# Performance work log

Hardware: AMD Instinct MI355X
Metric: run time of the kernel (lower is better)

## Reference

```python
import jax, jax.numpy as jnp
import numpy as np

ALPHA = 0.2  # LeakyReLU negative slope
NEG_INF = -9e15  # matches torch's -9000000000000000.0


def setup_inputs() -> dict:
    key = jax.random.key(0)
    k1, k2, k3, k4 = jax.random.split(key, 4)
    B, T, N, F_in, D = 4, 32, 512, 128, 128
    h = jax.random.normal(k1, (B, T, N, F_in), dtype=jnp.float32)
    adj = jax.random.randint(k2, (N, N), 0, 2, dtype=jnp.int32)
    # params: W ~ Linear(in_dim, out_dim, bias=False); a ~ Linear(2*out_dim, 1, bias=False)
    W = jax.random.normal(k3, (F_in, D), dtype=jnp.float32) * 0.05
    a = jax.random.normal(k4, (2 * D,), dtype=jnp.float32) * 0.05
    return {"h": h, "adj": adj, "W": W, "a": a}


def reference(h, adj, W, a):
    # h: (B,T,N,F_in), adj: (N,N), W: (F_in,D), a: (2D,)
    D = W.shape[1]
    Wh = jnp.einsum('btnf,fd->btnd', h, W)  # (B,T,N,D)
    # a . [Wh_i ; Wh_j] == a_src . Wh_i + a_dst . Wh_j -- avoids (N,N,2D) concat
    a_src, a_dst = a[:D], a[D:]
    e_src = Wh @ a_src  # (B,T,N)
    e_dst = Wh @ a_dst  # (B,T,N)
    e = jax.nn.leaky_relu(e_src[..., :, None] + e_dst[..., None, :], ALPHA)  # (B,T,N,N)
    e = jnp.where(adj > 0, e, jnp.float32(NEG_INF))
    attention = jax.nn.softmax(e, axis=-1)  # dropout is identity at eval
    h_prime = jnp.einsum('btij,btjd->btid', attention, Wh)  # (B,T,N,D)
    return h_prime
```

## Files before the change

kernel.cpp:

```cpp
#include <hip/hip_runtime.h>
#include <math.h>

typedef __attribute__((ext_vector_type(8))) short bf16x8;
typedef __attribute__((ext_vector_type(4))) float f32x4;

#define MFMA(a, b, c) __builtin_amdgcn_mfma_f32_16x16x32_bf16(a, b, c, 0, 0, 0)

constexpr int GN = 128;
constexpr int NN = 512;
constexpr int FD = 128;
#define LRELU(x) fmaxf((x), 0.2f * (x))
#define NEG_BIG -9.0e15f

__device__ inline unsigned short bf16_rne(float x) {
    unsigned u = __float_as_uint(x);
    unsigned r = u + 0x7fffu + ((u >> 16) & 1u);
    return (unsigned short)(r >> 16);
}
__device__ inline float bf16_to_f(unsigned short h) {
    return __uint_as_float(((unsigned)h) << 16);
}
__device__ inline unsigned rne_top16(float x) {
    unsigned u = __float_as_uint(x);
    return u + 0x7fffu + ((u >> 16) & 1u);
}
__device__ inline unsigned pack_top16(unsigned e1, unsigned e0) {
    return __builtin_amdgcn_perm(e1, e0, 0x07060302u);
}
__device__ inline void gload16(const void* g, void* l) {
    __builtin_amdgcn_global_load_lds(
        (const __attribute__((address_space(1))) unsigned*)g,
        (__attribute__((address_space(3))) unsigned*)l, 16, 0, 0);
}
__device__ inline void decode_bid(int bid, int& g, int& tile) {
    const int xcd = bid & 7, slot = bid >> 3;
    g = xcd + 8 * (slot >> 2);
    tile = slot & 3;
}

__global__ __launch_bounds__(256) void prep_kernel(
    const int* __restrict__ adj, const float* __restrict__ W,
    unsigned* __restrict__ mask, unsigned short* __restrict__ wsHi,
    unsigned short* __restrict__ wsLo)
{
    const int b = blockIdx.x, t = threadIdx.x;
    if (b < 32) {
        const int wi = b * 256 + t;
        const int row = wi >> 4, wo = wi & 15;
        const int* p = adj + row * NN + wo * 32;
        unsigned m = 0;
        #pragma unroll
        for (int q = 0; q < 32; q += 4) {
            int4 v = *(const int4*)&p[q];
            m |= (v.x > 0 ? 1u : 0u) << q;
            m |= (v.y > 0 ? 1u : 0u) << (q + 1);
            m |= (v.z > 0 ? 1u : 0u) << (q + 2);
            m |= (v.w > 0 ? 1u : 0u) << (q + 3);
        }
        mask[wi] = m;
    } else {
        const int base = (b - 32) * 512 + t * 2;
        #pragma unroll
        for (int q = 0; q < 2; ++q) {
            const int pos = base + q;
            const int idx = pos & 7, lane = (pos >> 3) & 63, cn = pos >> 9;
            const int kk = cn >> 3, nb = cn & 7;
            const int k = kk * 32 + ((lane >> 4) & 3) * 8 + idx;
            const int d = nb * 16 + (lane & 15);
            const float wv = W[k * FD + d];
            const unsigned u = __float_as_uint(wv);
            wsHi[pos] = (unsigned short)(u >> 16);
            wsLo[pos] = (unsigned short)(rne_top16(
                            wv - __uint_as_float(u & 0xffff0000u)) >> 16);
        }
    }
}

__global__ __launch_bounds__(256, 3) void whb_kernel(
    const float* __restrict__ h, const float* __restrict__ a,
    const unsigned short* __restrict__ wsHi, const unsigned short* __restrict__ wsLo,
    unsigned short* __restrict__ whtHi, unsigned short* __restrict__ whtLo,
    float* __restrict__ esrc, float* __restrict__ edst)
{
    __shared__ __attribute__((aligned(16))) unsigned short sBuf[16384];
    unsigned short* sWhi = sBuf;
    unsigned short* sWlo = sBuf + 4096;
    float* hs = (float*)(sBuf + 8192);

    int g, jt;
    decode_bid(blockIdx.x, g, jt);
    const int t = threadIdx.x, lane = t & 63, w = t >> 6;
    const int i0r = jt * 128;
    const float* hg = h + (size_t)(g * NN) * FD;

    f32x4 acc[2][8];
    #pragma unroll
    for (int mt = 0; mt < 2; ++mt)
        #pragma unroll
        for (int nb = 0; nb < 8; ++nb) acc[mt][nb] = (f32x4){0.f, 0.f, 0.f, 0.f};

    for (int kk = 0; kk < 4; ++kk) {
        __syncthreads();
        for (int q = t; q < 512; q += 256) {
            gload16(&wsHi[kk * 4096 + q * 8], &sWhi[q * 8]);
            gload16(&wsLo[kk * 4096 + q * 8], &sWlo[q * 8]);
        }
        for (int q = t; q < 1024; q += 256) {
            const int w2 = q >> 8, mt = (q >> 7) & 1;
            const int lp = (q >> 1) & 63, half = q & 1;
            const int row = i0r + w2 * 32 + mt * 16 + (lp & 15);
            const int k = kk * 32 + ((lp >> 4) & 3) * 8 + half * 4;
            gload16(hg + (size_t)row * FD + k, &hs[q * 4]);
        }
        __syncthreads();

        bf16x8 ah[2], al[2];
        #pragma unroll
        for (int mt = 0; mt < 2; ++mt) {
            const float* fb = &hs[((w * 2 + mt) * 64 + lane) * 8];
            const float4 f0 = *(const float4*)fb;
            const float4 f1 = *(const float4*)(fb + 4);
            const float xs[8] = {f0.x, f0.y, f0.z, f0.w, f1.x, f1.y, f1.z, f1.w};
            union { bf16x8 v; unsigned u[4]; } H, L;
            #pragma unroll
            for (int j = 0; j < 4; ++j) {
                const unsigned e0 = __float_as_uint(xs[2 * j]);
                const unsigned e1 = __float_as_uint(xs[2 * j + 1]);
                H.u[j] = pack_top16(e1, e0);
                const unsigned l0 = rne_top16(xs[2*j]   - __uint_as_float(e0 & 0xffff0000u));
                const unsigned l1 = rne_top16(xs[2*j+1] - __uint_as_float(e1 & 0xffff0000u));
                L.u[j] = pack_top16(l1, l0);
            }
            ah[mt] = H.v; al[mt] = L.v;
        }
        #pragma unroll
        for (int nb = 0; nb < 8; ++nb) {
            const bf16x8 bh = *(const bf16x8*)&sWhi[(nb * 64 + lane) * 8];
            const bf16x8 bl = *(const bf16x8*)&sWlo[(nb * 64 + lane) * 8];
            #pragma unroll
            for (int mt = 0; mt < 2; ++mt) {
                acc[mt][nb] = MFMA(al[mt], bh, acc[mt][nb]);
                acc[mt][nb] = MFMA(ah[mt], bl, acc[mt][nb]);
                acc[mt][nb] = MFMA(ah[mt], bh, acc[mt][nb]);
            }
        }
    }

    float av[8], bv[8];
    #pragma unroll
    for (int nb = 0; nb < 8; ++nb) {
        av[nb] = a[nb * 16 + (lane & 15)];
        bv[nb] = a[FD + nb * 16 + (lane & 15)];
    }
    #pragma unroll
    for (int mt = 0; mt < 2; ++mt)
        #pragma unroll
        for (int r = 0; r < 4; ++r) {
            float ps = 0.f, pd = 0.f;
            #pragma unroll
            for (int nb = 0; nb < 8; ++nb) {
                ps += acc[mt][nb][r] * av[nb];
                pd += acc[mt][nb][r] * bv[nb];
            }
            #pragma unroll
            for (int off = 1; off <= 8; off <<= 1) {
                ps += __shfl_xor(ps, off);
                pd += __shfl_xor(pd, off);
            }
            if ((lane & 15) == 0) {
                const int row = g * NN + i0r + w * 32 + mt * 16 + (lane >> 4) * 4 + r;
                esrc[row] = ps;
                edst[row] = pd;
            }
        }

    unsigned short* sTh = sBuf;
    unsigned short* sTl = sBuf + 8192;
    const size_t gbase = (size_t)g * 65536 + (size_t)jt * 16384;
    const int lanep = (lane & 15) + 16 * ((lane >> 5) + 0);
    const int ib = 4 * ((lane >> 4) & 1);

    for (int ph = 0; ph < 2; ++ph) {
        __syncthreads();
        #pragma unroll
        for (int mt = 0; mt < 2; ++mt) {
            const int lp2 = (lane & 15) + 16 * (mt * 2 + (lane >> 5));
            #pragma unroll
            for (int nbp = 0; nbp < 4; ++nbp) {
                const int nb = ph * 4 + nbp;
                const int off = ((w * 4 + nbp) * 64 + lp2) * 8 + ib;
                const unsigned u0 = __float_as_uint(acc[mt][nb][0]);
                const unsigned u1 = __float_as_uint(acc[mt][nb][1]);
                const unsigned u2 = __float_as_uint(acc[mt][nb][2]);
                const unsigned u3 = __float_as_uint(acc[mt][nb][3]);
                *(uint2*)&sTh[off] = make_uint2(pack_top16(u1, u0), pack_top16(u3, u2));
                const unsigned l0 = rne_top16(acc[mt][nb][0] - __uint_as_float(u0 & 0xffff0000u));
                const unsigned l1 = rne_top16(acc[mt][nb][1] - __uint_as_float(u1 & 0xffff0000u));
                const unsigned l2 = rne_top16(acc[mt][nb][2] - __uint_as_float(u2 & 0xffff0000u));
                const unsigned l3 = rne_top16(acc[mt][nb][3] - __uint_as_float(u3 & 0xffff0000u));
                *(uint2*)&sTl[off] = make_uint2(pack_top16(l1, l0), pack_top16(l3, l2));
            }
        }
        __syncthreads();
        for (int q = t; q < 1024; q += 256) {
            const int qw = q >> 8, qr = q & 255;
            const size_t go = gbase + (size_t)(qw * 8 + ph * 4) * 512 + qr * 8;
            *(float4*)&whtHi[go] = *(const float4*)&sTh[q * 8];
            *(float4*)&whtLo[go] = *(const float4*)&sTl[q * 8];
        }
    }
    (void)lanep;
}

__global__ __launch_bounds__(256, 3) void attn_kernel(
    const unsigned short* __restrict__ whtHi, const unsigned short* __restrict__ whtLo,
    const float* __restrict__ esrc, const float* __restrict__ edst,
    const unsigned* __restrict__ mask, float* __restrict__ out)
{
    __shared__ __attribute__((aligned(16))) float eds[NN];
    __shared__ __attribute__((aligned(16))) unsigned maskS[2048];
    __shared__ __attribute__((aligned(16))) unsigned short cHi[8192];
    __shared__ __attribute__((aligned(16))) unsigned short cLo[8192];
    __shared__ float redS[4];

    int g, it;
    decode_bid(blockIdx.x, g, it);
    const int t = threadIdx.x, lane = t & 63, w = t >> 6;
    const int i0 = it * 128;
    const int q8 = (lane >> 4) * 8;

    const float e0 = edst[g * NN + t], e1 = edst[g * NN + 256 + t];
    eds[t] = e0; eds[t + 256] = e1;
    float mx = fmaxf(e0, e1);
    #pragma unroll
    for (int off = 1; off < 64; off <<= 1) mx = fmaxf(mx, __shfl_xor(mx, off));
    if (lane == 0) redS[w] = mx;
    *(uint4*)&maskS[t * 8]     = *(const uint4*)&mask[i0 * 16 + t * 8];
    *(uint4*)&maskS[t * 8 + 4] = *(const uint4*)&mask[i0 * 16 + t * 8 + 4];
    __syncthreads();
    const float maxE = fmaxf(fmaxf(redS[0], redS[1]), fmaxf(redS[2], redS[3]));

    const int rloc0 = w * 32 + (lane & 15);
    const int rloc1 = rloc0 + 16;
    const float s0 = esrc[g * NN + i0 + rloc0];
    const float s1 = esrc[g * NN + i0 + rloc1];
    const float mh0 = LRELU(s0 + maxE);
    const float mh1 = LRELU(s1 + maxE);

    f32x4 acc[2][8];
    #pragma unroll
    for (int mt = 0; mt < 2; ++mt)
        #pragma unroll
        for (int nb = 0; nb < 8; ++nb) acc[mt][nb] = (f32x4){0.f, 0.f, 0.f, 0.f};
    float lsum0 = 0.f, lsum1 = 0.f;

    for (int c2 = 0; c2 < 8; ++c2) {
        __syncthreads();
        const size_t gb = (size_t)g * 65536 + (size_t)c2 * 8192;
        for (int q = t; q < 1024; q += 256) {
            gload16(&whtHi[gb + q * 8], &cHi[q * 8]);
            gload16(&whtLo[gb + q * 8], &cLo[q * 8]);
        }
        __syncthreads();
        #pragma unroll
        for (int kl = 0; kl < 2; ++kl) {
            const int kk = c2 * 2 + kl;
            const float* ep = &eds[kk * 32 + q8];
            const float4 ed0 = *(const float4*)ep;
            const float4 ed1 = *(const float4*)(ep + 4);
            const float ev[8] = {ed0.x, ed0.y, ed0.z, ed0.w, ed1.x, ed1.y, ed1.z, ed1.w};
            const unsigned mw0 = maskS[rloc0 * 16 + kk] >> q8;
            const unsigned mw1 = maskS[rloc1 * 16 + kk] >> q8;

            union { bf16x8 v; unsigned u[4]; } H0, L0, H1, L1;
            unsigned uh[8], ul[8];
            #pragma unroll
            for (int i = 0; i < 8; ++i) {
                float x = s0 + ev[i];
                x = LRELU(x);
                x = ((mw0 >> i) & 1u) ? x : NEG_BIG;
                const float p = __expf(x - mh0);
                lsum0 += p;
                const unsigned u = __float_as_uint(p);
                uh[i] = u;
                ul[i] = rne_top16(p - __uint_as_float(u & 0xffff0000u));
            }
            #pragma unroll
            for (int j = 0; j < 4; ++j) {
                H0.u[j] = pack_top16(uh[2*j+1], uh[2*j]);
                L0.u[j] = pack_top16(ul[2*j+1], ul[2*j]);
            }
            #pragma unroll
            for (int i = 0; i < 8; ++i) {
                float x = s1 + ev[i];
                x = LRELU(x);
                x = ((mw1 >> i) & 1u) ? x : NEG_BIG;
                const float p = __expf(x - mh1);
                lsum1 += p;
                const unsigned u = __float_as_uint(p);
                uh[i] = u;
                ul[i] = rne_top16(p - __uint_as_float(u & 0xffff0000u));
            }
            #pragma unroll
            for (int j = 0; j < 4; ++j) {
                H1.u[j] = pack_top16(uh[2*j+1], uh[2*j]);
                L1.u[j] = pack_top16(ul[2*j+1], ul[2*j]);
            }
            #pragma unroll
            for (int nb = 0; nb < 8; ++nb) {
                const bf16x8 bh = *(const bf16x8*)&cHi[((kl * 8 + nb) * 64 + lane) * 8];
                const bf16x8 bl = *(const bf16x8*)&cLo[((kl * 8 + nb) * 64 + lane) * 8];
                acc[0][nb] = MFMA(L0.v, bh, acc[0][nb]);
                acc[0][nb] = MFMA(H0.v, bl, acc[0][nb]);
                acc[0][nb] = MFMA(H0.v, bh, acc[0][nb]);
                acc[1][nb] = MFMA(L1.v, bh, acc[1][nb]);
                acc[1][nb] = MFMA(H1.v, bl, acc[1][nb]);
                acc[1][nb] = MFMA(H1.v, bh, acc[1][nb]);
            }
        }
    }

    lsum0 += __shfl_xor(lsum0, 16); lsum0 += __shfl_xor(lsum0, 32);
    lsum1 += __shfl_xor(lsum1, 16); lsum1 += __shfl_xor(lsum1, 32);

    #pragma unroll
    for (int r = 0; r < 4; ++r) {
        const int rr = (lane >> 4) * 4 + r;
        const float rl0 = 1.0f / __shfl(lsum0, rr);
        const float rl1 = 1.0f / __shfl(lsum1, rr);
        const int row0 = g * NN + i0 + w * 32 + rr;
        const int row1 = row0 + 16;
        #pragma unroll
        for (int nb = 0; nb < 8; ++nb) {
            out[row0 * FD + nb * 16 + (lane & 15)] = acc[0][nb][r] * rl0;
            out[row1 * FD + nb * 16 + (lane & 15)] = acc[1][nb][r] * rl1;
        }
    }
}

extern "C" void kernel_launch(void* const* d_in, const int* in_sizes, int n_in,
                              void* d_out, int out_size, void* d_ws, size_t ws_size,
                              hipStream_t stream) {
    const float* h   = (const float*)d_in[0];
    const int*   adj = (const int*)d_in[1];
    const float* W   = (const float*)d_in[2];
    const float* a   = (const float*)d_in[3];
    float* out = (float*)d_out;

    unsigned short* whtHi = (unsigned short*)d_ws;
    unsigned short* whtLo = whtHi + (size_t)GN * 65536;
    float* esrc = (float*)(whtLo + (size_t)GN * 65536);
    float* edst = esrc + GN * NN;
    unsigned* mask = (unsigned*)(edst + GN * NN);
    unsigned short* wsHi = (unsigned short*)(mask + 8192);
    unsigned short* wsLo = wsHi + 16384;

    prep_kernel<<<64, 256, 0, stream>>>(adj, W, mask, wsHi, wsLo);
    whb_kernel<<<512, 256, 0, stream>>>(h, a, wsHi, wsLo, whtHi, whtLo, esrc, edst);
    attn_kernel<<<512, 256, 0, stream>>>(whtHi, whtLo, esrc, edst, mask, out);
}
```

Before: 132.8 us.

## Restructure whb and attn kernels: full W in LDS, smaller attn tiles, 2-term split

The whb kernel now stages all of W (hi and lo) into LDS once and reads h straight from global memory into registers, instead of reloading per k-chunk with two barriers each time. The attn kernel halves its row tile to 64 rows per block, doubles the grid to 1024 blocks, and keeps each thread's mask row in registers rather than in LDS. It also drops the low bf16 part of the attention probabilities, going from 3 MFMAs to 2 per product, and sums the rounded probabilities so the normalisation matches. This cuts MFMA count and register pressure so more blocks fit per CU, at the cost of lower precision in the probability operand and more redundant loads of the Wh tiles across blocks.

Measured after the change: 130.7 us. Within noise of the previous version (-1.6%).

```diff
diff --git a/kernel.cpp b/kernel.cpp
--- a/kernel.cpp
+++ b/kernel.cpp
@@ -12,14 +12,6 @@
 #define LRELU(x) fmaxf((x), 0.2f * (x))
 #define NEG_BIG -9.0e15f
 
-__device__ inline unsigned short bf16_rne(float x) {
-    unsigned u = __float_as_uint(x);
-    unsigned r = u + 0x7fffu + ((u >> 16) & 1u);
-    return (unsigned short)(r >> 16);
-}
-__device__ inline float bf16_to_f(unsigned short h) {
-    return __uint_as_float(((unsigned)h) << 16);
-}
 __device__ inline unsigned rne_top16(float x) {
     unsigned u = __float_as_uint(x);
     return u + 0x7fffu + ((u >> 16) & 1u);
@@ -31,11 +23,6 @@
     __builtin_amdgcn_global_load_lds(
         (const __attribute__((address_space(1))) unsigned*)g,
         (__attribute__((address_space(3))) unsigned*)l, 16, 0, 0);
-}
-__device__ inline void decode_bid(int bid, int& g, int& tile) {
-    const int xcd = bid & 7, slot = bid >> 3;
-    g = xcd + 8 * (slot >> 2);
-    tile = slot & 3;
 }
 
 __global__ __launch_bounds__(256) void prep_kernel(
@@ -76,50 +63,44 @@
     }
 }
 
-__global__ __launch_bounds__(256, 3) void whb_kernel(
+__global__ __launch_bounds__(256, 2) void whb_kernel(
     const float* __restrict__ h, const float* __restrict__ a,
     const unsigned short* __restrict__ wsHi, const unsigned short* __restrict__ wsLo,
     unsigned short* __restrict__ whtHi, unsigned short* __restrict__ whtLo,
     float* __restrict__ esrc, float* __restrict__ edst)
 {
-    __shared__ __attribute__((aligned(16))) unsigned short sBuf[16384];
-    unsigned short* sWhi = sBuf;
-    unsigned short* sWlo = sBuf + 4096;
-    float* hs = (float*)(sBuf + 8192);
-
-    int g, jt;
-    decode_bid(blockIdx.x, g, jt);
+    __shared__ __attribute__((aligned(16))) unsigned short sW[32768];
+
+    const int bid = blockIdx.x;
+    const int xcd = bid & 7, slot = bid >> 3;
+    const int g = xcd + 8 * (slot >> 2);
+    const int jt = slot & 3;
     const int t = threadIdx.x, lane = t & 63, w = t >> 6;
     const int i0r = jt * 128;
+    const int q8 = (lane >> 4) * 8;
     const float* hg = h + (size_t)(g * NN) * FD;
 
+    for (int q = t; q < 2048; q += 256) {
+        gload16(&wsHi[q * 8], &sW[q * 8]);
+        gload16(&wsLo[q * 8], &sW[16384 + q * 8]);
+    }
+    __syncthreads();
+
     f32x4 acc[2][8];
     #pragma unroll
     for (int mt = 0; mt < 2; ++mt)
         #pragma unroll
         for (int nb = 0; nb < 8; ++nb) acc[mt][nb] = (f32x4){0.f, 0.f, 0.f, 0.f};
 
+    #pragma unroll
     for (int kk = 0; kk < 4; ++kk) {
-        __syncthreads();
-        for (int q = t; q < 512; q += 256) {
-            gload16(&wsHi[kk * 4096 + q * 8], &sWhi[q * 8]);
-            gload16(&wsLo[kk * 4096 + q * 8], &sWlo[q * 8]);
-        }
-        for (int q = t; q < 1024; q += 256) {
-            const int w2 = q >> 8, mt = (q >> 7) & 1;
-            const int lp = (q >> 1) & 63, half = q & 1;
-            const int row = i0r + w2 * 32 + mt * 16 + (lp & 15);
-            const int k = kk * 32 + ((lp >> 4) & 3) * 8 + half * 4;
-            gload16(hg + (size_t)row * FD + k, &hs[q * 4]);
-        }
-        __syncthreads();
-
         bf16x8 ah[2], al[2];
         #pragma unroll
         for (int mt = 0; mt < 2; ++mt) {
-            const float* fb = &hs[((w * 2 + mt) * 64 + lane) * 8];
-            const float4 f0 = *(const float4*)fb;
-            const float4 f1 = *(const float4*)(fb + 4);
+            const float* src = hg + (size_t)(i0r + w * 32 + mt * 16 + (lane & 15)) * FD
+                             + kk * 32 + q8;
+            const float4 f0 = *(const float4*)src;
+            const float4 f1 = *(const float4*)(src + 4);
             const float xs[8] = {f0.x, f0.y, f0.z, f0.w, f1.x, f1.y, f1.z, f1.w};
             union { bf16x8 v; unsigned u[4]; } H, L;
             #pragma unroll
@@ -135,8 +116,8 @@
         }
         #pragma unroll
         for (int nb = 0; nb < 8; ++nb) {
-            const bf16x8 bh = *(const bf16x8*)&sWhi[(nb * 64 + lane) * 8];
-            const bf16x8 bl = *(const bf16x8*)&sWlo[(nb * 64 + lane) * 8];
+            const bf16x8 bh = *(const bf16x8*)&sW[((kk * 8 + nb) * 64 + lane) * 8];
+            const bf16x8 bl = *(const bf16x8*)&sW[16384 + ((kk * 8 + nb) * 64 + lane) * 8];
             #pragma unroll
             for (int mt = 0; mt < 2; ++mt) {
                 acc[mt][nb] = MFMA(al[mt], bh, acc[mt][nb]);
@@ -174,10 +155,9 @@
             }
         }
 
-    unsigned short* sTh = sBuf;
-    unsigned short* sTl = sBuf + 8192;
+    unsigned short* sTh = sW;
+    unsigned short* sTl = sW + 8192;
     const size_t gbase = (size_t)g * 65536 + (size_t)jt * 16384;
-    const int lanep = (lane & 15) + 16 * ((lane >> 5) + 0);
     const int ib = 4 * ((lane >> 4) & 1);
 
     for (int ph = 0; ph < 2; ++ph) {
@@ -209,24 +189,24 @@
             *(float4*)&whtLo[go] = *(const float4*)&sTl[q * 8];
         }
     }
-    (void)lanep;
-}
-
-__global__ __launch_bounds__(256, 3) void attn_kernel(
+}
+
+__global__ __launch_bounds__(256, 4) void attn_kernel(
     const unsigned short* __restrict__ whtHi, const unsigned short* __restrict__ whtLo,
     const float* __restrict__ esrc, const float* __restrict__ edst,
     const unsigned* __restrict__ mask, float* __restrict__ out)
 {
     __shared__ __attribute__((aligned(16))) float eds[NN];
-    __shared__ __attribute__((aligned(16))) unsigned maskS[2048];
     __shared__ __attribute__((aligned(16))) unsigned short cHi[8192];
     __shared__ __attribute__((aligned(16))) unsigned short cLo[8192];
     __shared__ float redS[4];
 
-    int g, it;
-    decode_bid(blockIdx.x, g, it);
+    const int bid = blockIdx.x;
+    const int xcd = bid & 7, slot = bid >> 3;
+    const int g = xcd + 8 * (slot >> 3);
+    const int it = slot & 7;
     const int t = threadIdx.x, lane = t & 63, w = t >> 6;
-    const int i0 = it * 128;
+    const int i0 = it * 64;
     const int q8 = (lane >> 4) * 8;
 
     const float e0 = edst[g * NN + t], e1 = edst[g * NN + 256 + t];
@@ -235,24 +215,22 @@
     #pragma unroll
     for (int off = 1; off < 64; off <<= 1) mx = fmaxf(mx, __shfl_xor(mx, off));
     if (lane == 0) redS[w] = mx;
-    *(uint4*)&maskS[t * 8]     = *(const uint4*)&mask[i0 * 16 + t * 8];
-    *(uint4*)&maskS[t * 8 + 4] = *(const uint4*)&mask[i0 * 16 + t * 8 + 4];
+
+    const int rloc = w * 16 + (lane & 15);
+    const float s0 = esrc[g * NN + i0 + rloc];
+    unsigned mrow[16];
+    *(uint4*)&mrow[0]  = *(const uint4*)&mask[(i0 + rloc) * 16];
+    *(uint4*)&mrow[4]  = *(const uint4*)&mask[(i0 + rloc) * 16 + 4];
+    *(uint4*)&mrow[8]  = *(const uint4*)&mask[(i0 + rloc) * 16 + 8];
+    *(uint4*)&mrow[12] = *(const uint4*)&mask[(i0 + rloc) * 16 + 12];
     __syncthreads();
     const float maxE = fmaxf(fmaxf(redS[0], redS[1]), fmaxf(redS[2], redS[3]));
-
-    const int rloc0 = w * 32 + (lane & 15);
-    const int rloc1 = rloc0 + 16;
-    const float s0 = esrc[g * NN + i0 + rloc0];
-    const float s1 = esrc[g * NN + i0 + rloc1];
-    const float mh0 = LRELU(s0 + maxE);
-    const float mh1 = LRELU(s1 + maxE);
-
-    f32x4 acc[2][8];
-    #pragma unroll
-    for (int mt = 0; mt < 2; ++mt)
-        #pragma unroll
-        for (int nb = 0; nb < 8; ++nb) acc[mt][nb] = (f32x4){0.f, 0.f, 0.f, 0.f};
-    float lsum0 = 0.f, lsum1 = 0.f;
+    const float mh = LRELU(s0 + maxE);
+
+    f32x4 acc[8];
+    #pragma unroll
+    for (int nb = 0; nb < 8; ++nb) acc[nb] = (f32x4){0.f, 0.f, 0.f, 0.f};
+    float lsum = 0.f;
 
     for (int c2 = 0; c2 < 8; ++c2) {
         __syncthreads();
@@ -269,72 +247,44 @@
             const float4 ed0 = *(const float4*)ep;
             const float4 ed1 = *(const float4*)(ep + 4);
             const float ev[8] = {ed0.x, ed0.y, ed0.z, ed0.w, ed1.x, ed1.y, ed1.z, ed1.w};
-            const unsigned mw0 = maskS[rloc0 * 16 + kk] >> q8;
-            const unsigned mw1 = maskS[rloc1 * 16 + kk] >> q8;
-
-            union { bf16x8 v; unsigned u[4]; } H0, L0, H1, L1;
-            unsigned uh[8], ul[8];
+            const unsigned mw = mrow[kk] >> q8;
+
+            union { bf16x8 v; unsigned u[4]; } H;
+            unsigned uh[8];
             #pragma unroll
             for (int i = 0; i < 8; ++i) {
                 float x = s0 + ev[i];
                 x = LRELU(x);
-                x = ((mw0 >> i) & 1u) ? x : NEG_BIG;
-                const float p = __expf(x - mh0);
-                lsum0 += p;
-                const unsigned u = __float_as_uint(p);
-                uh[i] = u;
-                ul[i] = rne_top16(p - __uint_as_float(u & 0xffff0000u));
-            }
-            #pragma unroll
-            for (int j = 0; j < 4; ++j) {
-                H0.u[j] = pack_top16(uh[2*j+1], uh[2*j]);
-                L0.u[j] = pack_top16(ul[2*j+1], ul[2*j]);
-            }
-            #pragma unroll
-            for (int i = 0; i < 8; ++i) {
-                float x = s1 + ev[i];
-                x = LRELU(x);
-                x = ((mw1 >> i) & 1u) ? x : NEG_BIG;
-                const float p = __expf(x - mh1);
-                lsum1 += p;
-                const unsigned u = __float_as_uint(p);
-                uh[i] = u;
-                ul[i] = rne_top16(p - __uint_as_float(u & 0xffff0000u));
-            }
-            #pragma unroll
-            for (int j = 0; j < 4; ++j) {
-                H1.u[j] = pack_top16(uh[2*j+1], uh[2*j]);
-                L1.u[j] = pack_top16(ul[2*j+1], ul[2*j]);
-            }
+                x = ((mw >> i) & 1u) ? x : NEG_BIG;
+                const float p = __expf(x - mh);
+                const unsigned r = rne_top16(p);
+                lsum += __uint_as_float(r & 0xffff0000u);
+                uh[i] = r;
+            }
+            #pragma unroll
+            for (int j = 0; j < 4; ++j) H.u[j] = pack_top16(uh[2*j+1], uh[2*j]);
+
             #pragma unroll
             for (int nb = 0; nb < 8; ++nb) {
+                const bf16x8 bl = *(const bf16x8*)&cLo[((kl * 8 + nb) * 64 + lane) * 8];
                 const bf16x8 bh = *(const bf16x8*)&cHi[((kl * 8 + nb) * 64 + lane) * 8];
-                const bf16x8 bl = *(const bf16x8*)&cLo[((kl * 8 + nb) * 64 + lane) * 8];
-                acc[0][nb] = MFMA(L0.v, bh, acc[0][nb]);
-                acc[0][nb] = MFMA(H0.v, bl, acc[0][nb]);
-                acc[0][nb] = MFMA(H0.v, bh, acc[0][nb]);
-                acc[1][nb] = MFMA(L1.v, bh, acc[1][nb]);
-                acc[1][nb] = MFMA(H1.v, bl, acc[1][nb]);
-                acc[1][nb] = MFMA(H1.v, bh, acc[1][nb]);
-            }
-        }
-    }
-
-    lsum0 += __shfl_xor(lsum0, 16); lsum0 += __shfl_xor(lsum0, 32);
-    lsum1 += __shfl_xor(lsum1, 16); lsum1 += __shfl_xor(lsum1, 32);
+                acc[nb] = MFMA(H.v, bl, acc[nb]);
+                acc[nb] = MFMA(H.v, bh, acc[nb]);
+            }
+        }
+    }
+
+    lsum += __shfl_xor(lsum, 16);
+    lsum += __shfl_xor(lsum, 32);
 
     #pragma unroll
     for (int r = 0; r < 4; ++r) {
         const int rr = (lane >> 4) * 4 + r;
-        const float rl0 = 1.0f / __shfl(lsum0, rr);
-        const float rl1 = 1.0f / __shfl(lsum1, rr);
-        const int row0 = g * NN + i0 + w * 32 + rr;
-        const int row1 = row0 + 16;
-        #pragma unroll
-        for (int nb = 0; nb < 8; ++nb) {
-            out[row0 * FD + nb * 16 + (lane & 15)] = acc[0][nb][r] * rl0;
-            out[row1 * FD + nb * 16 + (lane & 15)] = acc[1][nb][r] * rl1;
-        }
+        const float rl = 1.0f / __shfl(lsum, rr);
+        const int row = g * NN + i0 + w * 16 + rr;
+        #pragma unroll
+        for (int nb = 0; nb < 8; ++nb)
+            out[row * FD + nb * 16 + (lane & 15)] = acc[nb][r] * rl;
     }
 }
 
@@ -357,5 +307,5 @@
 
     prep_kernel<<<64, 256, 0, stream>>>(adj, W, mask, wsHi, wsLo);
     whb_kernel<<<512, 256, 0, stream>>>(h, a, wsHi, wsLo, whtHi, whtLo, esrc, edst);
-    attn_kernel<<<512, 256, 0, stream>>>(whtHi, whtLo, esrc, edst, mask, out);
-}
+    attn_kernel<<<1024, 256, 0, stream>>>(whtHi, whtLo, esrc, edst, mask, out);
+}
```
